# Kernel optimization log

Hardware: AMD Instinct MI355X
Metric: run time of the kernel (lower is better)

Reference implementation:

```python
import jax, jax.numpy as jnp
import numpy as np

GROUP = 32  # values per quantization group (per-group scale)

def setup_inputs() -> dict:
    key = jax.random.key(0)
    k1, k2, k3, k4 = jax.random.split(key, 4)
    B, S, IN, OUT = 4, 2048, 4096, 4096
    x = jax.random.normal(k1, (B, S, IN), dtype=jnp.float32)
    # packed 4-bit weights: each int32 byte-value in [0,256) holds two nibbles
    w_packed = jax.random.randint(k2, (OUT, IN // 2), 0, 256, dtype=jnp.int32)
    scales = jax.random.uniform(k3, (OUT, IN // GROUP), dtype=jnp.float32) * 0.02 + 0.001
    bias = jax.random.normal(k4, (OUT,), dtype=jnp.float32)
    return {"x": x, "w_packed": w_packed, "scales": scales, "bias": bias}

def _dequantize(w_packed, scales):
    # w_packed: [OUT, IN//2] int32 bytes, scales: [OUT, IN//GROUP]
    OUT = w_packed.shape[0]
    low = w_packed & 0xF
    high = (w_packed >> 4) & 0xF
    q = jnp.stack([low, high], axis=-1).reshape(OUT, -1)  # [OUT, IN]
    qf = q.astype(jnp.float32) - 8.0  # signed 4-bit centered at 8
    qg = qf.reshape(OUT, scales.shape[1], GROUP)
    w = qg * scales[:, :, None]
    return w.reshape(OUT, -1)  # [OUT, IN]

def reference(x, w_packed, scales, bias):
    # dequantize weights then F.linear: y = x @ W^T + b
    W = _dequantize(w_packed, scales)  # [OUT, IN]
    y = jnp.einsum('bsi,oi->bso', x, W) + bias
    return y
```

## Files before the change

kernel.cpp:

```cpp
#include <hip/hip_runtime.h>
#include <stdint.h>

#define M_TOT 8192
#define K_TOT 4096
#define N_TOT 4096
#define GROUPQ 32

#define BM 256
#define BN 256
#define BK 64
#define NT (K_TOT / BK)

typedef __bf16 bf16x8 __attribute__((ext_vector_type(8)));
typedef float f32x4 __attribute__((ext_vector_type(4)));
typedef unsigned short u16;
typedef unsigned short u16x8 __attribute__((ext_vector_type(8)));

template <int V> struct IC { static constexpr int value = V; };

__device__ __forceinline__ u16 f2bf_rne(float f) {
  union { float f; uint32_t u; } v; v.f = f;
  uint32_t u = v.u;
  uint32_t r = (u + 0x7FFFu + ((u >> 16) & 1u)) >> 16;
  return (u16)r;
}

__global__ void prep_kernel(const float* __restrict__ x, const int* __restrict__ wp,
                            const float* __restrict__ sc,
                            u16* __restrict__ xb, u16* __restrict__ wb) {
  const int NCVT = M_TOT * K_TOT / 8;
  const int KH = K_TOT / 2;
  const int NDQ = N_TOT * KH / 8;
  int stride = gridDim.x * blockDim.x;
  int tid0 = blockIdx.x * blockDim.x + threadIdx.x;

  for (int i = tid0; i < NCVT; i += stride) {
    const float4* p = (const float4*)(x + (size_t)i * 8);
    float4 a = p[0];
    float4 b = p[1];
    u16x8 o;
    o[0] = f2bf_rne(a.x); o[1] = f2bf_rne(a.y); o[2] = f2bf_rne(a.z); o[3] = f2bf_rne(a.w);
    o[4] = f2bf_rne(b.x); o[5] = f2bf_rne(b.y); o[6] = f2bf_rne(b.z); o[7] = f2bf_rne(b.w);
    *(u16x8*)(xb + (size_t)i * 8) = o;
  }

  for (int t = tid0; t < NDQ; t += stride) {
    int base = t * 8;
    int o = base >> 11;
    int ci = base & 2047;
    int e0 = ci * 2;
    float scale = sc[o * (K_TOT / GROUPQ) + (e0 >> 5)];
    int4 p0 = *(const int4*)(wp + base);
    int4 p1 = *(const int4*)(wp + base + 4);
    int v[8] = {p0.x, p0.y, p0.z, p0.w, p1.x, p1.y, p1.z, p1.w};
    u16x8 oA, oB;
#pragma unroll
    for (int j = 0; j < 8; ++j) {
      float lo = (float)((v[j] & 0xF) - 8) * scale;
      float hi = (float)(((v[j] >> 4) & 0xF) - 8) * scale;
      u16 lob = f2bf_rne(lo), hib = f2bf_rne(hi);
      if (j < 4) { oA[2 * j] = lob; oA[2 * j + 1] = hib; }
      else       { oB[2 * (j - 4)] = lob; oB[2 * (j - 4) + 1] = hib; }
    }
    u16* dst = wb + (size_t)o * K_TOT + e0;
    *(u16x8*)dst = oA;
    *(u16x8*)(dst + 8) = oB;
  }
}

__global__ __launch_bounds__(512, 2) void gemm_bf16_kernel(
    const u16* __restrict__ A, const u16* __restrict__ Bt,
    const float* __restrict__ bias, float* __restrict__ C) {
  __shared__ alignas(16) u16 sL[65536];

  const int ntn = N_TOT / BN;
  int wg = blockIdx.x, nwg = gridDim.x;
  int cpx = nwg >> 3;
  int swz = (wg & 7) * cpx + (wg >> 3);
  int bm = swz / ntn, bn = swz % ntn;

  int tid = threadIdx.x, wid = tid >> 6, lane = tid & 63;
  int wr = wid >> 2, wc = wid & 3;
  const size_t K = K_TOT;

  int rowS = tid >> 2;
  int cgS = (tid & 3) ^ ((rowS >> 1) & 3);
  const u16* pA = A + ((size_t)(bm * 256 + (rowS >> 6) * 128 + (rowS & 63))) * K + cgS * 8;
  const u16* pB = Bt + ((size_t)(bn * 256 + (rowS >> 5) * 64 + (rowS & 31))) * K + cgS * 8;
  u16* sE = &sL[0];

#define GLLDS(src, dst)                                                      \
  __builtin_amdgcn_global_load_lds(                                          \
      (const __attribute__((address_space(1))) uint32_t*)(src),              \
      (__attribute__((address_space(3))) uint32_t*)(dst), 16, 0, 0)

  auto stA = [&](int T, int mh, auto bufc) {
    constexpr int buf = decltype(bufc)::value;
    const u16* s = pA + (size_t)mh * 64 * K + (size_t)T * 64;
    GLLDS(s,      sE + ((buf * 2 + 0) * 2 + mh) * 4096 + tid * 8);
    GLLDS(s + 32, sE + ((buf * 2 + 1) * 2 + mh) * 4096 + tid * 8);
  };
  auto stB = [&](int T, int nh, auto bufc) {
    constexpr int buf = decltype(bufc)::value;
    const u16* s = pB + (size_t)nh * 32 * K + (size_t)T * 64;
    GLLDS(s,      sE + 32768 + ((buf * 2 + 0) * 2 + nh) * 4096 + tid * 8);
    GLLDS(s + 32, sE + 32768 + ((buf * 2 + 1) * 2 + nh) * 4096 + tid * 8);
  };

  int rA = wr * 64 + (lane & 15);
  int cA = ((lane >> 4) ^ ((rA >> 1) & 3)) * 8;
  int rB = wc * 32 + (lane & 15);
  int cB = ((lane >> 4) ^ ((rB >> 1) & 3)) * 8;
  const u16* rdA = sE + rA * 32 + cA;
  const u16* rdB = sE + 32768 + rB * 32 + cB;
  auto ldA = [&](auto bufc, int kk, int mh, int m3) {
    constexpr int buf = decltype(bufc)::value;
    return *(const bf16x8*)(rdA + ((buf * 2 + kk) * 2 + mh) * 4096 + m3 * 16 * 32);
  };
  auto ldB = [&](auto bufc, int kk, int nh, int n2) {
    constexpr int buf = decltype(bufc)::value;
    return *(const bf16x8*)(rdB + ((buf * 2 + kk) * 2 + nh) * 4096 + n2 * 16 * 32);
  };

  f32x4 acc[8][4] = {};
  bf16x8 a0[4][2], a1[4][2], b0[2][2], b1[2][2];

  stA(0, 0, IC<0>{}); stB(0, 0, IC<0>{}); stB(0, 1, IC<0>{}); stA(0, 1, IC<0>{});
  stA(1, 0, IC<1>{}); stB(1, 0, IC<1>{}); stB(1, 1, IC<1>{}); stA(1, 1, IC<1>{});
  asm volatile("s_waitcnt vmcnt(4)" ::: "memory");
  __builtin_amdgcn_s_barrier();

#pragma unroll
  for (int m3 = 0; m3 < 4; ++m3)
#pragma unroll
    for (int kk = 0; kk < 2; ++kk) a0[m3][kk] = ldA(IC<0>{}, kk, 0, m3);
#pragma unroll
  for (int n2 = 0; n2 < 2; ++n2)
#pragma unroll
    for (int kk = 0; kk < 2; ++kk) b0[n2][kk] = ldB(IC<0>{}, kk, 0, n2);
  asm volatile("s_waitcnt lgkmcnt(0)" ::: "memory");
  __builtin_amdgcn_s_barrier();

  auto tile_body = [&](int t, auto bufc, auto nbufc) {
    bool st_ok = (t + 2 < NT);
    bool rd_ok = (t + 1 < NT);
    int Ts = t + 2;

#pragma unroll
    for (int n2 = 0; n2 < 2; ++n2)
#pragma unroll
      for (int kk = 0; kk < 2; ++kk) b1[n2][kk] = ldB(bufc, kk, 1, n2);
    if (st_ok) stA(Ts, 0, bufc);
    __builtin_amdgcn_s_setprio(1);
#pragma unroll
    for (int kk = 0; kk < 2; ++kk)
#pragma unroll
      for (int m3 = 0; m3 < 4; ++m3)
#pragma unroll
        for (int n2 = 0; n2 < 2; ++n2)
          acc[m3][n2] = __builtin_amdgcn_mfma_f32_16x16x32_bf16(a0[m3][kk], b0[n2][kk], acc[m3][n2], 0, 0, 0);
    __builtin_amdgcn_s_setprio(0);

#pragma unroll
    for (int m3 = 0; m3 < 4; ++m3)
#pragma unroll
      for (int kk = 0; kk < 2; ++kk) a1[m3][kk] = ldA(bufc, kk, 1, m3);
    if (st_ok) stB(Ts, 0, bufc);
    __builtin_amdgcn_s_setprio(1);
#pragma unroll
    for (int kk = 0; kk < 2; ++kk)
#pragma unroll
      for (int m3 = 0; m3 < 4; ++m3)
#pragma unroll
        for (int n2 = 0; n2 < 2; ++n2)
          acc[m3][n2 + 2] = __builtin_amdgcn_mfma_f32_16x16x32_bf16(a0[m3][kk], b1[n2][kk], acc[m3][n2 + 2], 0, 0, 0);
    __builtin_amdgcn_s_setprio(0);
    __builtin_amdgcn_s_barrier();

    if (rd_ok) {
#pragma unroll
      for (int m3 = 0; m3 < 4; ++m3)
#pragma unroll
        for (int kk = 0; kk < 2; ++kk) a0[m3][kk] = ldA(nbufc, kk, 0, m3);
    }
    if (st_ok) stB(Ts, 1, bufc);
    __builtin_amdgcn_s_setprio(1);
#pragma unroll
    for (int kk = 0; kk < 2; ++kk)
#pragma unroll
      for (int m3 = 0; m3 < 4; ++m3)
#pragma unroll
        for (int n2 = 0; n2 < 2; ++n2)
          acc[m3 + 4][n2] = __builtin_amdgcn_mfma_f32_16x16x32_bf16(a1[m3][kk], b0[n2][kk], acc[m3 + 4][n2], 0, 0, 0);
    __builtin_amdgcn_s_setprio(0);
    __builtin_amdgcn_s_barrier();

    if (rd_ok) {
#pragma unroll
      for (int n2 = 0; n2 < 2; ++n2)
#pragma unroll
        for (int kk = 0; kk < 2; ++kk) b0[n2][kk] = ldB(nbufc, kk, 0, n2);
    }
    if (st_ok) stA(Ts, 1, bufc);
    __builtin_amdgcn_s_setprio(1);
#pragma unroll
    for (int kk = 0; kk < 2; ++kk)
#pragma unroll
      for (int m3 = 0; m3 < 4; ++m3)
#pragma unroll
        for (int n2 = 0; n2 < 2; ++n2)
          acc[m3 + 4][n2 + 2] = __builtin_amdgcn_mfma_f32_16x16x32_bf16(a1[m3][kk], b1[n2][kk], acc[m3 + 4][n2 + 2], 0, 0, 0);
    __builtin_amdgcn_s_setprio(0);
    asm volatile("s_waitcnt lgkmcnt(0)" ::: "memory");
    if (t < NT - 2) { asm volatile("s_waitcnt vmcnt(4)" ::: "memory"); }
    else            { asm volatile("s_waitcnt vmcnt(0)" ::: "memory"); }
    __builtin_amdgcn_s_barrier();
  };

  for (int t = 0; t < NT; t += 2) {
    tile_body(t,     IC<0>{}, IC<1>{});
    tile_body(t + 1, IC<1>{}, IC<0>{});
  }

  asm volatile("s_waitcnt vmcnt(0)" ::: "memory");

  int col = lane & 15;
  int rb = (lane >> 4) * 4;
#pragma unroll
  for (int n = 0; n < 4; ++n) {
    int gn = bn * BN + wc * 64 + n * 16 + col;
    float bsv = bias[gn];
#pragma unroll
    for (int m = 0; m < 8; ++m) {
      int gm = bm * BM + wr * 128 + m * 16 + rb;
#pragma unroll
      for (int j = 0; j < 4; ++j)
        C[(size_t)(gm + j) * N_TOT + gn] = acc[m][n][j] + bsv;
    }
  }
#undef GLLDS
}

__global__ void fill_kernel(float* p, int n, float v) {
  int stride = gridDim.x * blockDim.x;
  for (int i = blockIdx.x * blockDim.x + threadIdx.x; i < n; i += stride) p[i] = v;
}

extern "C" void kernel_launch(void* const* d_in, const int* in_sizes, int n_in,
                              void* d_out, int out_size, void* d_ws, size_t ws_size,
                              hipStream_t stream) {
  const float* x = (const float*)d_in[0];
  const int* wp = (const int*)d_in[1];
  const float* sc = (const float*)d_in[2];
  const float* bias = (const float*)d_in[3];
  float* out = (float*)d_out;

  size_t xb_bytes = (size_t)M_TOT * K_TOT * 2;
  size_t wb_bytes = (size_t)N_TOT * K_TOT * 2;
  if (ws_size < xb_bytes + wb_bytes) {
    fill_kernel<<<2048, 256, 0, stream>>>(out, out_size, 12345.0f);
    return;
  }
  u16* xb = (u16*)d_ws;
  u16* wb = (u16*)((char*)d_ws + xb_bytes);

  prep_kernel<<<2048, 256, 0, stream>>>(x, wp, sc, xb, wb);
  gemm_bf16_kernel<<<(M_TOT / BM) * (N_TOT / BN), 512, 0, stream>>>(xb, wb, bias, out);
}
```

Baseline: 266.6 us.

## Restructure GEMM main loop into staggered 8-wave ping-pong schedule

Reworks the double-buffered main loop so each quarter-tile loads its own fragments from LDS at the start of the phase rather than prefetching the next tile's fragments. Global-to-LDS stores are interleaved per phase with finer vmcnt/lgkmcnt waits and extra barriers. Out-of-range tiles are clamped to the last tile instead of guarded by branches, which removes divergent control flow but issues redundant loads. The aim is to overlap memory and MFMA work more evenly across waves, at the cost of more barriers and less register prefetch.

```diff
diff --git a/kernel.cpp b/kernel.cpp
--- a/kernel.cpp
+++ b/kernel.cpp
@@ -125,65 +125,64 @@
   f32x4 acc[8][4] = {};
   bf16x8 a0[4][2], a1[4][2], b0[2][2], b1[2][2];
 
-  stA(0, 0, IC<0>{}); stB(0, 0, IC<0>{}); stB(0, 1, IC<0>{}); stA(0, 1, IC<0>{});
-  stA(1, 0, IC<1>{}); stB(1, 0, IC<1>{}); stB(1, 1, IC<1>{}); stA(1, 1, IC<1>{});
+  stA(0, 0, IC<0>{}); stB(0, 0, IC<0>{}); stA(0, 1, IC<0>{}); stB(0, 1, IC<0>{});
   asm volatile("s_waitcnt vmcnt(4)" ::: "memory");
+  stA(1, 0, IC<1>{}); stB(1, 0, IC<1>{}); stA(1, 1, IC<1>{});
+  asm volatile("s_waitcnt vmcnt(6)" ::: "memory");
   __builtin_amdgcn_s_barrier();
 
-#pragma unroll
-  for (int m3 = 0; m3 < 4; ++m3)
-#pragma unroll
-    for (int kk = 0; kk < 2; ++kk) a0[m3][kk] = ldA(IC<0>{}, kk, 0, m3);
-#pragma unroll
-  for (int n2 = 0; n2 < 2; ++n2)
-#pragma unroll
-    for (int kk = 0; kk < 2; ++kk) b0[n2][kk] = ldB(IC<0>{}, kk, 0, n2);
-  asm volatile("s_waitcnt lgkmcnt(0)" ::: "memory");
-  __builtin_amdgcn_s_barrier();
-
   auto tile_body = [&](int t, auto bufc, auto nbufc) {
-    bool st_ok = (t + 2 < NT);
-    bool rd_ok = (t + 1 < NT);
-    int Ts = t + 2;
-
+    int Tc1 = (t + 1 < NT) ? t + 1 : NT - 1;
+    int Tc2 = (t + 2 < NT) ? t + 2 : NT - 1;
+
+#pragma unroll
+    for (int m3 = 0; m3 < 4; ++m3)
+#pragma unroll
+      for (int kk = 0; kk < 2; ++kk) a0[m3][kk] = ldA(bufc, kk, 0, m3);
 #pragma unroll
     for (int n2 = 0; n2 < 2; ++n2)
 #pragma unroll
+      for (int kk = 0; kk < 2; ++kk) b0[n2][kk] = ldB(bufc, kk, 0, n2);
+    stB(Tc1, 1, nbufc);
+    asm volatile("s_waitcnt lgkmcnt(8)" ::: "memory");
+    __builtin_amdgcn_s_barrier();
+    asm volatile("s_waitcnt lgkmcnt(0)" ::: "memory");
+    __builtin_amdgcn_s_setprio(1);
+#pragma unroll
+    for (int kk = 0; kk < 2; ++kk)
+#pragma unroll
+      for (int m3 = 0; m3 < 4; ++m3)
+#pragma unroll
+        for (int n2 = 0; n2 < 2; ++n2)
+          acc[m3][n2] = __builtin_amdgcn_mfma_f32_16x16x32_bf16(a0[m3][kk], b0[n2][kk], acc[m3][n2], 0, 0, 0);
+    __builtin_amdgcn_s_setprio(0);
+    __builtin_amdgcn_s_barrier();
+
+#pragma unroll
+    for (int n2 = 0; n2 < 2; ++n2)
+#pragma unroll
       for (int kk = 0; kk < 2; ++kk) b1[n2][kk] = ldB(bufc, kk, 1, n2);
-    if (st_ok) stA(Ts, 0, bufc);
-    __builtin_amdgcn_s_setprio(1);
-#pragma unroll
-    for (int kk = 0; kk < 2; ++kk)
-#pragma unroll
-      for (int m3 = 0; m3 < 4; ++m3)
-#pragma unroll
-        for (int n2 = 0; n2 < 2; ++n2)
-          acc[m3][n2] = __builtin_amdgcn_mfma_f32_16x16x32_bf16(a0[m3][kk], b0[n2][kk], acc[m3][n2], 0, 0, 0);
-    __builtin_amdgcn_s_setprio(0);
+    stA(Tc2, 0, bufc);
+    __builtin_amdgcn_s_barrier();
+    asm volatile("s_waitcnt lgkmcnt(0)" ::: "memory");
+    __builtin_amdgcn_s_setprio(1);
+#pragma unroll
+    for (int kk = 0; kk < 2; ++kk)
+#pragma unroll
+      for (int m3 = 0; m3 < 4; ++m3)
+#pragma unroll
+        for (int n2 = 0; n2 < 2; ++n2)
+          acc[m3][n2 + 2] = __builtin_amdgcn_mfma_f32_16x16x32_bf16(a0[m3][kk], b1[n2][kk], acc[m3][n2 + 2], 0, 0, 0);
+    __builtin_amdgcn_s_setprio(0);
+    __builtin_amdgcn_s_barrier();
 
 #pragma unroll
     for (int m3 = 0; m3 < 4; ++m3)
 #pragma unroll
       for (int kk = 0; kk < 2; ++kk) a1[m3][kk] = ldA(bufc, kk, 1, m3);
-    if (st_ok) stB(Ts, 0, bufc);
-    __builtin_amdgcn_s_setprio(1);
-#pragma unroll
-    for (int kk = 0; kk < 2; ++kk)
-#pragma unroll
-      for (int m3 = 0; m3 < 4; ++m3)
-#pragma unroll
-        for (int n2 = 0; n2 < 2; ++n2)
-          acc[m3][n2 + 2] = __builtin_amdgcn_mfma_f32_16x16x32_bf16(a0[m3][kk], b1[n2][kk], acc[m3][n2 + 2], 0, 0, 0);
-    __builtin_amdgcn_s_setprio(0);
-    __builtin_amdgcn_s_barrier();
-
-    if (rd_ok) {
-#pragma unroll
-      for (int m3 = 0; m3 < 4; ++m3)
-#pragma unroll
-        for (int kk = 0; kk < 2; ++kk) a0[m3][kk] = ldA(nbufc, kk, 0, m3);
-    }
-    if (st_ok) stB(Ts, 1, bufc);
+    stB(Tc2, 0, bufc);
+    __builtin_amdgcn_s_barrier();
+    asm volatile("s_waitcnt lgkmcnt(0)" ::: "memory");
     __builtin_amdgcn_s_setprio(1);
 #pragma unroll
     for (int kk = 0; kk < 2; ++kk)
@@ -195,13 +194,9 @@
     __builtin_amdgcn_s_setprio(0);
     __builtin_amdgcn_s_barrier();
 
-    if (rd_ok) {
-#pragma unroll
-      for (int n2 = 0; n2 < 2; ++n2)
-#pragma unroll
-        for (int kk = 0; kk < 2; ++kk) b0[n2][kk] = ldB(nbufc, kk, 0, n2);
-    }
-    if (st_ok) stA(Ts, 1, bufc);
+    stA(Tc2, 1, bufc);
+    asm volatile("s_waitcnt vmcnt(6)" ::: "memory");
+    __builtin_amdgcn_s_barrier();
     __builtin_amdgcn_s_setprio(1);
 #pragma unroll
     for (int kk = 0; kk < 2; ++kk)
@@ -211,9 +206,6 @@
         for (int n2 = 0; n2 < 2; ++n2)
           acc[m3 + 4][n2 + 2] = __builtin_amdgcn_mfma_f32_16x16x32_bf16(a1[m3][kk], b1[n2][kk], acc[m3 + 4][n2 + 2], 0, 0, 0);
     __builtin_amdgcn_s_setprio(0);
-    asm volatile("s_waitcnt lgkmcnt(0)" ::: "memory");
-    if (t < NT - 2) { asm volatile("s_waitcnt vmcnt(4)" ::: "memory"); }
-    else            { asm volatile("s_waitcnt vmcnt(0)" ::: "memory"); }
     __builtin_amdgcn_s_barrier();
   };
 
```

New measurement: 269.7 us. About the same (+1.2%).
